# Kernel tuning notes

Measured on AMD Instinct MI355X. Metric: run time of the kernel, lower is better.

Reference implementation:

```python
import jax, jax.numpy as jnp
import numpy as np

N_HEADS = 16
ROPE_BASE = 10000.0


def _rope_cos_sin(seq_len, head_dim, dtype):
    half = head_dim // 2
    inv_freq = 1.0 / (ROPE_BASE ** (jnp.arange(0, half, dtype=jnp.float32) / half))
    ang = jnp.arange(seq_len, dtype=jnp.float32)[:, None] * inv_freq[None, :]  # [S, half]
    cos = jnp.concatenate([jnp.cos(ang), jnp.cos(ang)], axis=-1).astype(dtype)  # [S, hd]
    sin = jnp.concatenate([jnp.sin(ang), jnp.sin(ang)], axis=-1).astype(dtype)
    return cos, sin


def _rotate_half(x):
    half = x.shape[-1] // 2
    return jnp.concatenate([-x[..., half:], x[..., :half]], axis=-1)


def setup_inputs() -> dict:
    key = jax.random.key(0)
    k1, k2, k3 = jax.random.split(key, 3)
    B, S, D = 2, 2048, 1024
    x = jax.random.normal(k1, (B, S, D), dtype=jnp.float32)
    w_qkv = jax.random.normal(k2, (D, 3 * D), dtype=jnp.float32) * (1.0 / np.sqrt(D))
    w_out = jax.random.normal(k3, (D, D), dtype=jnp.float32) * (1.0 / np.sqrt(D))
    return {"x": x, "w_qkv": w_qkv, "w_out": w_out}


def reference(x, w_qkv, w_out):
    B, S, D = x.shape
    H = N_HEADS
    hd = D // H
    scale = 1.0 / np.sqrt(hd)

    qkv = x @ w_qkv  # [B, S, 3D]
    q, k, v = jnp.split(qkv, 3, axis=-1)
    # [B, H, S, hd]
    q = q.reshape(B, S, H, hd).transpose(0, 2, 1, 3)
    k = k.reshape(B, S, H, hd).transpose(0, 2, 1, 3)
    v = v.reshape(B, S, H, hd).transpose(0, 2, 1, 3)

    cos, sin = _rope_cos_sin(S, hd, x.dtype)  # [S, hd]
    q = q * cos + _rotate_half(q) * sin
    k = k * cos + _rotate_half(k) * sin

    scores = jnp.einsum("bhqd,bhkd->bhqk", q, k) * scale  # [B, H, S, S]
    causal = jnp.tril(jnp.ones((S, S), dtype=bool))
    scores = jnp.where(causal[None, None, :, :], scores, -jnp.inf)

    probs = jax.nn.softmax(scores.astype(jnp.float32), axis=-1).astype(q.dtype)
    out = jnp.einsum("bhqk,bhkd->bhqd", probs, v)  # [B, H, S, hd]
    out = out.transpose(0, 2, 1, 3).reshape(B, S, D)
    return out @ w_out
```

## Files before the change

### kernel.cpp

```cpp
#include <hip/hip_runtime.h>
#include <math.h>
#include <type_traits>

#define B_  2
#define S_  2048
#define D_  1024
#define H_  16

typedef short bf16x8 __attribute__((ext_vector_type(8)));
typedef short bf16x4 __attribute__((ext_vector_type(4)));
typedef float f32x4  __attribute__((ext_vector_type(4)));

__device__ __forceinline__ short f2bf(float f) {
    unsigned u = __builtin_bit_cast(unsigned, f);
    u += 0x7FFFu + ((u >> 16) & 1u);
    return (short)(u >> 16);
}
__device__ __forceinline__ float bf2f(short s) {
    unsigned u = ((unsigned)(unsigned short)s) << 16;
    return __builtin_bit_cast(float, u);
}

__device__ __forceinline__ void gload16(const short* g, const void* l) {
    __builtin_amdgcn_global_load_lds(
        (const __attribute__((address_space(1))) void*)g,
        (__attribute__((address_space(3))) void*)l, 16, 0, 0);
}

__global__ __launch_bounds__(256) void cvt_bf16_kernel(
    const float* __restrict__ in, short* __restrict__ out)
{
    int i = (blockIdx.x * 256 + threadIdx.x) * 8;
    float4 a = *(const float4*)(in + i);
    float4 b = *(const float4*)(in + i + 4);
    bf16x8 o;
    o[0] = f2bf(a.x); o[1] = f2bf(a.y); o[2] = f2bf(a.z); o[3] = f2bf(a.w);
    o[4] = f2bf(b.x); o[5] = f2bf(b.y); o[6] = f2bf(b.z); o[7] = f2bf(b.w);
    *(bf16x8*)(out + i) = o;
}

__global__ __launch_bounds__(256) void transpose_cvt_kernel(
    const float* __restrict__ in, short* __restrict__ out, int K, int N)
{
    __shared__ short t[64][72];
    const int k0 = blockIdx.y * 64, n0 = blockIdx.x * 64;
    const int r = threadIdx.x >> 2;
    const int c = (threadIdx.x & 3) * 16;
    const float* src = in + (size_t)(k0 + r) * N + n0 + c;
#pragma unroll
    for (int i = 0; i < 16; ++i) t[c + i][r] = f2bf(src[i]);
    __syncthreads();
    short* dst = out + (size_t)(n0 + r) * K + k0 + c;
    *(bf16x8*)(dst)     = *(const bf16x8*)&t[r][c];
    *(bf16x8*)(dst + 8) = *(const bf16x8*)&t[r][c + 8];
}

__global__ __launch_bounds__(256) void rope_tab_kernel(float2* __restrict__ tab)
{
    int idx = blockIdx.x * 256 + threadIdx.x;
    int j = idx & 31, s = idx >> 5;
    float inv = powf(10000.0f, -(float)j * (1.0f / 32.0f));
    float sn, cs;
    sincosf((float)s * inv, &sn, &cs);
    tab[idx] = make_float2(cs, sn);
}

__global__ __launch_bounds__(256) void gemm_bt_f32(
    const short* __restrict__ A, const short* __restrict__ Bt,
    float* __restrict__ C, int M, int N, int K)
{
    __shared__ short As[128 * 32];
    __shared__ short Bs[64 * 32];

    const int tid  = threadIdx.x;
    const int wave = tid >> 6, lane = tid & 63;
    const int quad = lane >> 4, l16 = lane & 15;
    const int wm = wave >> 1, wn = wave & 1;
    const int row0 = blockIdx.y * 128, col0 = blockIdx.x * 64;

    f32x4 acc[4][2];
#pragma unroll
    for (int mi = 0; mi < 4; ++mi)
#pragma unroll
        for (int ni = 0; ni < 2; ++ni) acc[mi][ni] = (f32x4)0.f;

    const int sr = tid >> 2;
    const int sc = (tid & 3) * 8;
    const short* a0 = A  + (size_t)(row0 + sr) * K + sc;
    const short* a1 = A  + (size_t)(row0 + 64 + sr) * K + sc;
    const short* b0 = Bt + (size_t)(col0 + sr) * K + sc;
    char* lA0 = (char*)As + wave * 1024;
    char* lA1 = (char*)As + 4096 + wave * 1024;
    char* lB0 = (char*)Bs + wave * 1024;

    for (int k0 = 0; k0 < K; k0 += 32) {
        __syncthreads();
        gload16(a0 + k0, lA0);
        gload16(a1 + k0, lA1);
        gload16(b0 + k0, lB0);
        __syncthreads();

        bf16x8 af[4], bfr[2];
#pragma unroll
        for (int mi = 0; mi < 4; ++mi)
            af[mi] = *(const bf16x8*)(As + (wm * 64 + mi * 16 + l16) * 32 + quad * 8);
#pragma unroll
        for (int ni = 0; ni < 2; ++ni)
            bfr[ni] = *(const bf16x8*)(Bs + (wn * 32 + ni * 16 + l16) * 32 + quad * 8);
#pragma unroll
        for (int mi = 0; mi < 4; ++mi)
#pragma unroll
            for (int ni = 0; ni < 2; ++ni)
                acc[mi][ni] = __builtin_amdgcn_mfma_f32_16x16x32_bf16(
                    af[mi], bfr[ni], acc[mi][ni], 0, 0, 0);
    }

#pragma unroll
    for (int mi = 0; mi < 4; ++mi)
#pragma unroll
        for (int ni = 0; ni < 2; ++ni)
#pragma unroll
            for (int r = 0; r < 4; ++r) {
                int row = row0 + wm * 64 + mi * 16 + quad * 4 + r;
                int col = col0 + wn * 32 + ni * 16 + l16;
                C[(size_t)row * N + col] = acc[mi][ni][r];
            }
}

__global__ __launch_bounds__(256) void gemm_qkv(
    const short* __restrict__ A, const short* __restrict__ Bt,
    const float2* __restrict__ tab,
    short* __restrict__ Qb, short* __restrict__ Kb, short* __restrict__ Vt)
{
    const int K = 1024;
    extern __shared__ short smem[];
    short* As = smem;
    short* Bs = smem + 4096;
    short* Sc = smem;

    const int tid  = threadIdx.x;
    const int wave = tid >> 6, lane = tid & 63;
    const int quad = lane >> 4, l16 = lane & 15;
    const int wm = wave >> 1, wn = wave & 1;
    const int row0 = blockIdx.y * 128, col0 = blockIdx.x * 128;

    f32x4 acc[4][4];
#pragma unroll
    for (int mi = 0; mi < 4; ++mi)
#pragma unroll
        for (int ni = 0; ni < 4; ++ni) acc[mi][ni] = (f32x4)0.f;

    const int sr = tid >> 2;
    const int sc = (tid & 3) * 8;
    const short* a0 = A  + (size_t)(row0 + sr) * K + sc;
    const short* a1 = A  + (size_t)(row0 + 64 + sr) * K + sc;
    const short* b0 = Bt + (size_t)(col0 + sr) * K + sc;
    const short* b1 = Bt + (size_t)(col0 + 64 + sr) * K + sc;
    char* lA0 = (char*)As + wave * 1024;
    char* lA1 = (char*)As + 4096 + wave * 1024;
    char* lB0 = (char*)Bs + wave * 1024;
    char* lB1 = (char*)Bs + 4096 + wave * 1024;

    for (int k0 = 0; k0 < K; k0 += 32) {
        __syncthreads();
        gload16(a0 + k0, lA0);
        gload16(a1 + k0, lA1);
        gload16(b0 + k0, lB0);
        gload16(b1 + k0, lB1);
        __syncthreads();

        bf16x8 af[4], bfr[4];
#pragma unroll
        for (int mi = 0; mi < 4; ++mi)
            af[mi] = *(const bf16x8*)(As + (wm * 64 + mi * 16 + l16) * 32 + quad * 8);
#pragma unroll
        for (int ni = 0; ni < 4; ++ni)
            bfr[ni] = *(const bf16x8*)(Bs + (wn * 64 + ni * 16 + l16) * 32 + quad * 8);
#pragma unroll
        for (int mi = 0; mi < 4; ++mi)
#pragma unroll
            for (int ni = 0; ni < 4; ++ni)
                acc[mi][ni] = __builtin_amdgcn_mfma_f32_16x16x32_bf16(
                    af[mi], bfr[ni], acc[mi][ni], 0, 0, 0);
    }

    __syncthreads();

    const int sec  = (col0 + wn * 64) >> 6;
    const int h    = sec & 15;
    const int kind = sec >> 4;
    short* myS = Sc + wave * 4608;

    const int mrow0 = row0 + wm * 64;
    const int b  = mrow0 >> 11;
    const int bh = b * 16 + h;
    const int sbase = mrow0 & (S_ - 1);

    if (kind < 2) {
#pragma unroll
        for (int mi = 0; mi < 4; ++mi) {
#pragma unroll
            for (int r = 0; r < 4; ++r) {
                int sl = mi * 16 + quad * 4 + r;
                int s = sbase + sl;
#pragma unroll
                for (int ni = 0; ni < 2; ++ni) {
                    int j = ni * 16 + l16;
                    float2 t = tab[s * 32 + j];
                    float lo = acc[mi][ni][r], hi = acc[mi][ni + 2][r];
                    float olo = lo * t.x - hi * t.y;
                    float ohi = hi * t.x + lo * t.y;
                    if (kind == 0) { olo *= 0.125f; ohi *= 0.125f; }
                    myS[sl * 72 + j]      = f2bf(olo);
                    myS[sl * 72 + 32 + j] = f2bf(ohi);
                }
            }
        }
        const int rl = lane >> 3;
        const int cl = (lane & 7) * 8;
        if (kind == 0) {
#pragma unroll
            for (int p = 0; p < 8; ++p) {
                int rr = p * 8 + rl;
                bf16x8 v = *(const bf16x8*)&myS[rr * 72 + cl];
                *(bf16x8*)(Qb + ((size_t)bh * S_ + sbase + rr) * 64 + cl) = v;
            }
        } else {
#pragma unroll
            for (int p = 0; p < 8; ++p) {
                int rr = p * 8 + rl;
                bf16x8 v = *(const bf16x8*)&myS[rr * 72 + cl];
                *(bf16x8*)(Kb + ((size_t)bh * S_ + sbase + rr) * 72 + cl) = v;
            }
        }
    } else {
#pragma unroll
        for (int mi = 0; mi < 4; ++mi)
#pragma unroll
            for (int ni = 0; ni < 4; ++ni) {
                bf16x4 p;
                p[0] = f2bf(acc[mi][ni][0]);
                p[1] = f2bf(acc[mi][ni][1]);
                p[2] = f2bf(acc[mi][ni][2]);
                p[3] = f2bf(acc[mi][ni][3]);
                *(bf16x4*)&myS[(ni * 16 + l16) * 72 + mi * 16 + quad * 4] = p;
            }
        const int rl = lane >> 3;
        const int cl = (lane & 7) * 8;
#pragma unroll
        for (int p = 0; p < 8; ++p) {
            int dd = p * 8 + rl;
            bf16x8 v = *(const bf16x8*)&myS[dd * 72 + cl];
            *(bf16x8*)(Vt + ((size_t)bh * 64 + dd) * S_ + sbase + cl) = v;
        }
    }
}

__global__ __launch_bounds__(256) void attn_kernel(
    const short* __restrict__ Qb, const short* __restrict__ Kb,
    const short* __restrict__ Vt, short* __restrict__ Opart,
    float* __restrict__ lpart)
{
    __shared__ short Ks[2][64 * 72];
    __shared__ short Vs[2][64 * 72];
    __shared__ short Ps[64][72];

    const int lin = blockIdx.x;
    const int xcd = lin & 7;
    const int j   = lin >> 3;
    const int bh   = xcd * 4 + (j & 3);
    const int task = j >> 2;

    const int g = task < 8 ? 0 : task < 24 ? 1 : task < 48 ? 2 : 3;
    const int cumstart = g == 0 ? 0 : g == 1 ? 8 : g == 2 ? 24 : 48;
    const int idx = task - cumstart;
    const int qd = idx / (g + 1);
    const int qb = 8 * g + qd;
    const int c  = idx - qd * (g + 1);
    const int t0 = c * 8;
    const int t1 = min(qb, c * 8 + 7);

    const int wave = threadIdx.x >> 6, lane = threadIdx.x & 63;
    const int quad = lane >> 4, l16 = lane & 15;
    const size_t head64 = (size_t)bh * S_ * 64;
    const size_t headK  = (size_t)bh * S_ * 72;

    const short* qrow = Qb + head64
        + (size_t)(qb * 64 + wave * 16 + l16) * 64 + quad * 8;
    const bf16x8 qf0 = *(const bf16x8*)(qrow);
    const bf16x8 qf1 = *(const bf16x8*)(qrow + 32);

    bf16x8 ones;
#pragma unroll
    for (int i = 0; i < 8; ++i) ones[i] = (short)0x3F80;

    int vr[3], vc[3];
#pragma unroll
    for (int u = 0; u < 3; ++u) {
        int jj = wave + u * 4;
        int e = jj * 64 + lane;
        vr[u] = e / 9;
        vc[u] = e * 8 - vr[u] * 72;
    }

    auto stageKV = [&](int buf, int t) {
        const short* kt  = Kb + headK + (size_t)t * 4608;
        const short* vtb = Vt + head64 + t * 64;
        short* kl = Ks[buf];
        short* vl = Vs[buf];
#pragma unroll
        for (int u = 0; u < 3; ++u) {
            int jj = wave + u * 4;
            if (jj < 9) {
                gload16(kt + jj * 512 + lane * 8, (char*)kl + jj * 1024);
                gload16(vtb + (size_t)vr[u] * S_ + vc[u], (char*)vl + jj * 1024);
            }
        }
    };

    f32x4 lacc = (f32x4)0.f;
    f32x4 oacc[4];
#pragma unroll
    for (int nt = 0; nt < 4; ++nt) oacc[nt] = (f32x4)0.f;

    int buf = 0;
    stageKV(0, t0);
    for (int t = t0; t <= t1; ++t) {
        __syncthreads();
        if (t < t1) stageKV(buf ^ 1, t + 1);

        const short* kb = Ks[buf];
        const short* vb = Vs[buf];

        f32x4 s4[4];
#pragma unroll
        for (int nt = 0; nt < 4; ++nt) {
            const short* kr = kb + (nt * 16 + l16) * 72 + quad * 8;
            bf16x8 b0 = *(const bf16x8*)kr;
            bf16x8 b1 = *(const bf16x8*)(kr + 32);
            f32x4 a = (f32x4)0.f;
            a = __builtin_amdgcn_mfma_f32_16x16x32_bf16(qf0, b0, a, 0, 0, 0);
            a = __builtin_amdgcn_mfma_f32_16x16x32_bf16(qf1, b1, a, 0, 0, 0);
            s4[nt] = a;
        }

        if (t == qb) {
#pragma unroll
            for (int nt = 0; nt < 4; ++nt)
#pragma unroll
                for (int r = 0; r < 4; ++r)
                    if (nt * 16 + l16 > wave * 16 + quad * 4 + r)
                        s4[nt][r] = -INFINITY;
        }

#pragma unroll
        for (int nt = 0; nt < 4; ++nt)
#pragma unroll
            for (int r = 0; r < 4; ++r)
                Ps[wave * 16 + quad * 4 + r][nt * 16 + l16] =
                    f2bf(__expf(s4[nt][r] - 8.0f));

        bf16x8 pa0 = *(const bf16x8*)&Ps[wave * 16 + l16][quad * 8];
        bf16x8 pa1 = *(const bf16x8*)&Ps[wave * 16 + l16][32 + quad * 8];
        lacc = __builtin_amdgcn_mfma_f32_16x16x32_bf16(pa0, ones, lacc, 0, 0, 0);
        lacc = __builtin_amdgcn_mfma_f32_16x16x32_bf16(pa1, ones, lacc, 0, 0, 0);
#pragma unroll
        for (int nt = 0; nt < 4; ++nt) {
            const short* vrp = vb + (nt * 16 + l16) * 72 + quad * 8;
            bf16x8 vb0 = *(const bf16x8*)vrp;
            bf16x8 vb1 = *(const bf16x8*)(vrp + 32);
            oacc[nt] = __builtin_amdgcn_mfma_f32_16x16x32_bf16(
                pa0, vb0, oacc[nt], 0, 0, 0);
            oacc[nt] = __builtin_amdgcn_mfma_f32_16x16x32_bf16(
                pa1, vb1, oacc[nt], 0, 0, 0);
        }
        buf ^= 1;
    }

    const int pidx = bh * 80 + task;
#pragma unroll
    for (int r = 0; r < 4; ++r) {
        int ql = wave * 16 + quad * 4 + r;
        short* orow = Opart + (size_t)pidx * 4096 + ql * 64;
#pragma unroll
        for (int nt = 0; nt < 4; ++nt)
            orow[nt * 16 + l16] = f2bf(oacc[nt][r]);
        if (l16 == 0)
            lpart[(size_t)pidx * 64 + ql] = lacc[r];
    }
}

__global__ __launch_bounds__(256) void combine_kernel(
    const short* __restrict__ Opart, const float* __restrict__ lpart,
    short* __restrict__ attnb)
{
    const int qb = blockIdx.x, bh = blockIdx.y;
    const int g = qb >> 3, nch = g + 1;
    const int cbase = bh * 80 + nch * (qb - 4 * g);
    const int q = threadIdx.x >> 2;
    const int dg = (threadIdx.x & 3) * 16;

    float lsum = 0.f;
    float acc[16];
#pragma unroll
    for (int i = 0; i < 16; ++i) acc[i] = 0.f;

    for (int cc = 0; cc < nch; ++cc) {
        lsum += lpart[(size_t)(cbase + cc) * 64 + q];
        const short* src = Opart + (size_t)(cbase + cc) * 4096 + q * 64 + dg;
        bf16x8 o0 = *(const bf16x8*)src;
        bf16x8 o1 = *(const bf16x8*)(src + 8);
#pragma unroll
        for (int i = 0; i < 8; ++i) {
            acc[i]     += bf2f(o0[i]);
            acc[i + 8] += bf2f(o1[i]);
        }
    }
    float inv = 1.0f / lsum;
    const int b = bh >> 4, h = bh & 15;
    bf16x8 r0, r1;
#pragma unroll
    for (int i = 0; i < 8; ++i) {
        r0[i] = f2bf(acc[i] * inv);
        r1[i] = f2bf(acc[i + 8] * inv);
    }
    short* dst = attnb + (size_t)(b * S_ + qb * 64 + q) * 1024 + h * 64 + dg;
    *(bf16x8*)dst       = r0;
    *(bf16x8*)(dst + 8) = r1;
}

extern "C" void kernel_launch(void* const* d_in, const int* in_sizes, int n_in,
                              void* d_out, int out_size, void* d_ws, size_t ws_size,
                              hipStream_t stream)
{
    const float* x     = (const float*)d_in[0];
    const float* w_qkv = (const float*)d_in[1];
    const float* w_out = (const float*)d_in[2];
    float* out = (float*)d_out;

    short* Qb   = (short*)d_ws;
    short* Kb   = Qb   + (size_t)4096 * 1024;
    short* Vt   = Kb   + (size_t)32 * 2048 * 72;
    short* Xb   = Vt   + (size_t)4096 * 1024;
    short* Wqt  = Xb   + (size_t)4096 * 1024;
    short* Wot  = Wqt  + (size_t)3072 * 1024;
    float2* tab = (float2*)(Wot + (size_t)1024 * 1024);
    short* Opart = (short*)(tab + 2048 * 32);
    float* lbuf  = (float*)(Opart + (size_t)2560 * 4096);
    short* attnb = Xb;

    cvt_bf16_kernel<<<(4096 * 1024 / 8) / 256, 256, 0, stream>>>(x, Xb);
    transpose_cvt_kernel<<<dim3(3072 / 64, 1024 / 64), 256, 0, stream>>>(
        w_qkv, Wqt, 1024, 3072);
    transpose_cvt_kernel<<<dim3(1024 / 64, 1024 / 64), 256, 0, stream>>>(
        w_out, Wot, 1024, 1024);
    rope_tab_kernel<<<(2048 * 32) / 256, 256, 0, stream>>>(tab);

    gemm_qkv<<<dim3(3072 / 128, 4096 / 128), 256, 36864, stream>>>(
        Xb, Wqt, tab, Qb, Kb, Vt);

    attn_kernel<<<2560, 256, 0, stream>>>(Qb, Kb, Vt, Opart, lbuf);

    combine_kernel<<<dim3(32, 32), 256, 0, stream>>>(Opart, lbuf, attnb);

    gemm_bt_f32<<<dim3(1024 / 64, 4096 / 128), 256, 0, stream>>>(
        attnb, Wot, out, 4096, 1024, 1024);
}
```

Baseline: 205.8 us.

## Triple-buffer LDS loads in both GEMMs with vmcnt-based waits

Both GEMM kernels replace the load, sync, compute loop with a three-stage LDS ring buffer. Global-to-LDS loads for tile k+2 are issued while tile k is computed. Each iteration uses a partial s_waitcnt vmcnt plus a single barrier instead of two __syncthreads. This is meant to hide global memory latency behind MFMA work, at the cost of more LDS per block (49152 bytes for gemm_qkv, 36 KB for the output GEMM), which may reduce occupancy.

```diff
diff --git a/kernel.cpp b/kernel.cpp
--- a/kernel.cpp
+++ b/kernel.cpp
@@ -69,8 +69,7 @@
     const short* __restrict__ A, const short* __restrict__ Bt,
     float* __restrict__ C, int M, int N, int K)
 {
-    __shared__ short As[128 * 32];
-    __shared__ short Bs[64 * 32];
+    __shared__ short smem[18432];
 
     const int tid  = threadIdx.x;
     const int wave = tid >> 6, lane = tid & 63;
@@ -89,17 +88,31 @@
     const short* a0 = A  + (size_t)(row0 + sr) * K + sc;
     const short* a1 = A  + (size_t)(row0 + 64 + sr) * K + sc;
     const short* b0 = Bt + (size_t)(col0 + sr) * K + sc;
-    char* lA0 = (char*)As + wave * 1024;
-    char* lA1 = (char*)As + 4096 + wave * 1024;
-    char* lB0 = (char*)Bs + wave * 1024;
-
-    for (int k0 = 0; k0 < K; k0 += 32) {
-        __syncthreads();
-        gload16(a0 + k0, lA0);
-        gload16(a1 + k0, lA1);
-        gload16(b0 + k0, lB0);
-        __syncthreads();
-
+
+    auto stage = [&](int b, int kt) {
+        char* l = (char*)(smem + b * 6144) + wave * 1024;
+        const int k0 = kt * 32;
+        gload16(a0 + k0, l);
+        gload16(a1 + k0, l + 4096);
+        gload16(b0 + k0, l + 8192);
+    };
+
+    const int NT = K >> 5;
+    stage(0, 0);
+    stage(1, 1);
+    int bufid = 0;
+    for (int kt = 0; kt < NT; ++kt) {
+        if (kt + 1 < NT) { asm volatile("s_waitcnt vmcnt(3)" ::: "memory"); }
+        else             { asm volatile("s_waitcnt vmcnt(0)" ::: "memory"); }
+        __builtin_amdgcn_s_barrier();
+        __builtin_amdgcn_sched_barrier(0);
+        if (kt + 2 < NT) {
+            int nb = bufid + 2; if (nb >= 3) nb -= 3;
+            stage(nb, kt + 2);
+        }
+
+        const short* As = smem + bufid * 6144;
+        const short* Bs = As + 4096;
         bf16x8 af[4], bfr[2];
 #pragma unroll
         for (int mi = 0; mi < 4; ++mi)
@@ -113,6 +126,8 @@
             for (int ni = 0; ni < 2; ++ni)
                 acc[mi][ni] = __builtin_amdgcn_mfma_f32_16x16x32_bf16(
                     af[mi], bfr[ni], acc[mi][ni], 0, 0, 0);
+
+        bufid = (bufid + 1 == 3) ? 0 : bufid + 1;
     }
 
 #pragma unroll
@@ -134,8 +149,6 @@
 {
     const int K = 1024;
     extern __shared__ short smem[];
-    short* As = smem;
-    short* Bs = smem + 4096;
     short* Sc = smem;
 
     const int tid  = threadIdx.x;
@@ -156,19 +169,32 @@
     const short* a1 = A  + (size_t)(row0 + 64 + sr) * K + sc;
     const short* b0 = Bt + (size_t)(col0 + sr) * K + sc;
     const short* b1 = Bt + (size_t)(col0 + 64 + sr) * K + sc;
-    char* lA0 = (char*)As + wave * 1024;
-    char* lA1 = (char*)As + 4096 + wave * 1024;
-    char* lB0 = (char*)Bs + wave * 1024;
-    char* lB1 = (char*)Bs + 4096 + wave * 1024;
-
-    for (int k0 = 0; k0 < K; k0 += 32) {
-        __syncthreads();
-        gload16(a0 + k0, lA0);
-        gload16(a1 + k0, lA1);
-        gload16(b0 + k0, lB0);
-        gload16(b1 + k0, lB1);
-        __syncthreads();
-
+
+    auto stage = [&](int b, int kt) {
+        char* l = (char*)(smem + b * 8192) + wave * 1024;
+        const int k0 = kt * 32;
+        gload16(a0 + k0, l);
+        gload16(a1 + k0, l + 4096);
+        gload16(b0 + k0, l + 8192);
+        gload16(b1 + k0, l + 12288);
+    };
+
+    const int NT = K >> 5;
+    stage(0, 0);
+    stage(1, 1);
+    int bufid = 0;
+    for (int kt = 0; kt < NT; ++kt) {
+        if (kt + 1 < NT) { asm volatile("s_waitcnt vmcnt(4)" ::: "memory"); }
+        else             { asm volatile("s_waitcnt vmcnt(0)" ::: "memory"); }
+        __builtin_amdgcn_s_barrier();
+        __builtin_amdgcn_sched_barrier(0);
+        if (kt + 2 < NT) {
+            int nb = bufid + 2; if (nb >= 3) nb -= 3;
+            stage(nb, kt + 2);
+        }
+
+        const short* As = smem + bufid * 8192;
+        const short* Bs = As + 4096;
         bf16x8 af[4], bfr[4];
 #pragma unroll
         for (int mi = 0; mi < 4; ++mi)
@@ -182,6 +208,8 @@
             for (int ni = 0; ni < 4; ++ni)
                 acc[mi][ni] = __builtin_amdgcn_mfma_f32_16x16x32_bf16(
                     af[mi], bfr[ni], acc[mi][ni], 0, 0, 0);
+
+        bufid = (bufid + 1 == 3) ? 0 : bufid + 1;
     }
 
     __syncthreads();
@@ -456,7 +484,7 @@
         w_out, Wot, 1024, 1024);
     rope_tab_kernel<<<(2048 * 32) / 256, 256, 0, stream>>>(tab);
 
-    gemm_qkv<<<dim3(3072 / 128, 4096 / 128), 256, 36864, stream>>>(
+    gemm_qkv<<<dim3(3072 / 128, 4096 / 128), 256, 49152, stream>>>(
         Xb, Wqt, tab, Qb, Kb, Vt);
 
     attn_kernel<<<2560, 256, 0, stream>>>(Qb, Kb, Vt, Opart, lbuf);
```

Result: faster. 187.0 us (-9.2%).
